# Optimization experiments

Hardware: AMD Instinct MI355X
Metric: run time of the kernel (lower is better)

## Reference

```python
import jax, jax.numpy as jnp
import numpy as np

LAG = 13
B = 32
N = 1200
NUM = 0  # self.num at call time (module starts at the init value)
H = 1.0 / 3.0


def gamma_fn(x):
    # Gamma function valid for positive and negative non-integer args
    # (reflection formula for x<0), elementwise, fp32-safe.
    xp = jnp.where(x > 0, x, jnp.float32(1.0))
    pos = jnp.exp(jax.lax.lgamma(xp))
    xn = jnp.where(x > 0, jnp.float32(0.5), x)
    neg = jnp.pi / (jnp.sin(jnp.pi * xn) * jnp.exp(jax.lax.lgamma(1.0 - xn)))
    return jnp.where(x > 0, pos, neg)


def aggregate(A, WW):
    # Fused form of: repeat_interleave -> view -> mul(WW) -> sum(dim=2) -> tanh(-x)
    # v0[l,b,i,j,e] = A[l,b,i,e]; out[l,b,j,e] = tanh(-sum_i WW[i,j,e]*A[l,b,i,e])
    return jnp.tanh(-jnp.einsum('lbie,ije->lbje', A, WW))


def setup_inputs() -> dict:
    key = jax.random.key(0)
    k = jax.random.split(key, 7)
    A = jax.random.normal(k[0], (LAG - 1, B, N, 1), jnp.float32)
    WW = jax.random.normal(k[1], (N, N, 1), jnp.float32) * 0.03
    train_init = jax.random.uniform(k[2], (B, N, LAG, 2), jnp.float32)
    alpha = jax.random.uniform(k[3], (LAG - 1, 1), jnp.float32) * 0.6 + 0.2
    fract = jax.random.uniform(k[4], (LAG - 1, 1), jnp.float32) * 0.6 + 0.2
    lambd = jax.random.normal(k[5], (LAG - 1, 1, N // 6, 1), jnp.float32) * 0.1
    l = jax.random.normal(k[6], (LAG - 1, 1, N // 6, 1), jnp.float32) * 0.1
    A_y_list = jnp.zeros((12, B, LAG - 1, N, 1), jnp.float32)
    return {"A": A, "WW": WW, "train_init": train_init, "alpha": alpha,
            "fract": fract, "lambd": lambd, "l": l, "A_y_list": A_y_list}


def reference(A, WW, train_init, alpha, fract, lambd, l, A_y_list):
    # __init__-time precomputation of A_N_OLD / A_0_NEW
    A_N_OLD = aggregate(jnp.transpose(train_init[..., :LAG - 1, 1], (2, 0, 1))[..., None], WW)
    A_0_NEW = aggregate(jnp.transpose(train_init[..., 1:LAG, 1], (2, 0, 1))[..., None], WW)

    out = aggregate(A, WW)                                   # [lag-1,B,N,1]
    A_y_list = A_y_list.at[NUM].set(jnp.transpose(out, (1, 0, 2, 3)))

    # D(): the original overwrites num=0 inside D, so only the m=0 GL term
    # survives; binom(fract,0)=Gamma(f+1)/(Gamma(1)Gamma(f+1)).
    binom0 = gamma_fn(fract + 1.0) / (gamma_fn(jnp.ones_like(fract)) * gamma_fn(fract + 1.0))
    sum_GL = A_y_list[0] * binom0[None, :, None, :]          # [B,lag-1,N,1]
    output_final_A = sum_GL / (H ** fract[None, :, None, :])

    # belta_result = sum_{k=0..3} Gamma(a+1)/(Gamma(k+1)Gamma(a-k+1))
    g_a1 = gamma_fn(alpha + 1.0)                             # [lag-1,1]
    belta_result = jnp.zeros((LAG - 1, 1), jnp.float32)
    for kk in range(4):
        kf = jnp.full((LAG - 1, 1), float(kk), jnp.float32)
        belta_result = belta_result + g_a1 / (gamma_fn(kf + 1.0) * gamma_fn(alpha - kf + 1.0))

    tmp1 = g_a1[:, None, None, :]                            # Gamma(a+1), == tmp3
    tmp2 = gamma_fn(jnp.ones((LAG - 1, 1), jnp.float32))[:, None, None, :]   # Gamma(1)=1
    tmp4 = gamma_fn(jnp.full((LAG - 1, 1), 4.0, jnp.float32))[:, None, None, :]  # Gamma(4)=6
    tmp5 = gamma_fn(alpha - 2.0)[:, None, None, :]           # Gamma(a-3+1)

    l_rep = jnp.tile(l, (1, B, 6, 1))                        # [lag-1,B,N,1]
    constant = l_rep * (tmp1 / (tmp2 * tmp1) * A_0_NEW + tmp1 / (tmp4 * tmp5) * A_N_OLD) / H
    constant = jnp.transpose(constant, (1, 0, 2, 3))         # [B,lag-1,N,1]

    lambd_rep = jnp.transpose(jnp.tile(lambd, (1, B, 6, 1)), (1, 0, 2, 3))
    return lambd_rep / belta_result[None, :, None, :] * (2.0 * output_final_A + constant)
```

## Files before the change

kernel.cpp:

```cpp
#include <hip/hip_runtime.h>
#include <math.h>

#define PI_F 3.14159265358979323846f

typedef __attribute__((ext_vector_type(8))) short bh8;
typedef __attribute__((ext_vector_type(4))) float f32x4;

#define LAG1 12
#define BB   32
#define NN   1200
#define MROWS 1152
#define KPAD 1216
#define NPAD 1216

__device__ __forceinline__ unsigned short f2bf(float f) {
    unsigned int u = __float_as_uint(f);
    u = (u + 0x7fffu + ((u >> 16) & 1u)) >> 16;
    return (unsigned short)u;
}

__device__ __forceinline__ float gamma_fn_dev(float x) {
    if (x > 0.0f) return expf(lgammaf(x));
    return PI_F / (sinf(PI_F * x) * expf(lgammaf(1.0f - x)));
}

__global__ void prep_coef(const float* __restrict__ alpha, const float* __restrict__ fract,
                          float* __restrict__ coef) {
    int lag = threadIdx.x;
    if (lag >= LAG1) return;
    float a = alpha[lag], f = fract[lag];
    float ga1 = expf(lgammaf(a + 1.0f));
    float belta = 0.0f;
    const float gk[4] = {1.0f, 1.0f, 2.0f, 6.0f};
    #pragma unroll
    for (int kk = 0; kk < 4; kk++)
        belta += ga1 / (gk[kk] * gamma_fn_dev(a - (float)kk + 1.0f));
    float c2 = ga1 / (6.0f * gamma_fn_dev(a - 2.0f));
    coef[lag]      = 2.0f * powf(3.0f, f);
    coef[12 + lag] = c2;
    coef[24 + lag] = 1.0f / belta;
}

__global__ void prep_X(const float* __restrict__ A, const float* __restrict__ TI,
                       unsigned short* __restrict__ X) {
    int idx = blockIdx.x * 256 + threadIdx.x;
    if (idx >= MROWS * KPAD) return;
    int r = idx / KPAD, k = idx - r * KPAD;
    float v = 0.0f;
    if (k < NN) {
        int g = r / 384, rr = r - g * 384;
        int lag = rr >> 5, b = rr & 31;
        if (g == 0) {
            v = A[rr * NN + k];
        } else {
            int lg = (g == 1) ? lag : (lag + 1);
            v = TI[((b * NN + k) * 13 + lg) * 2 + 1];
        }
    }
    X[idx] = f2bf(v);
}

__global__ void prep_WT(const float* __restrict__ WW, unsigned short* __restrict__ WT) {
    __shared__ float tile[32][33];
    int i0 = blockIdx.y * 32, j0 = blockIdx.x * 32;
    int tx = threadIdx.x, ty = threadIdx.y;
    #pragma unroll
    for (int s = 0; s < 32; s += 8) {
        int i = i0 + ty + s, j = j0 + tx;
        tile[ty + s][tx] = (i < NN && j < NN) ? WW[i * NN + j] : 0.0f;
    }
    __syncthreads();
    #pragma unroll
    for (int s = 0; s < 32; s += 8) {
        int j = j0 + ty + s, i = i0 + tx;
        WT[j * NPAD + i] = f2bf(tile[tx][ty + s]);
    }
}

__global__ __launch_bounds__(256) void gemm_kernel(const unsigned short* __restrict__ X,
                                                   const unsigned short* __restrict__ WT,
                                                   float* __restrict__ T) {
    __shared__ unsigned short As[64 * 40];
    __shared__ unsigned short Bs[64 * 40];
    const int tid  = threadIdx.x;
    const int bm   = blockIdx.x, bn = blockIdx.y;
    const int wave = tid >> 6, lane = tid & 63;
    const int wm   = (wave >> 1) * 32, wn = (wave & 1) * 32;
    const int lrow = tid >> 2;
    const int lcol = (tid & 3) * 8;
    const int l15  = lane & 15;
    const int kq   = (lane >> 4) * 8;

    const unsigned short* gA = X  + (bm * 64 + lrow) * KPAD + lcol;
    const unsigned short* gB = WT + (bn * 64 + lrow) * NPAD + lcol;

    f32x4 acc[2][2] = {};

    for (int k0 = 0; k0 < KPAD; k0 += 32) {
        __syncthreads();
        *(int4*)&As[lrow * 40 + lcol] = *(const int4*)(gA + k0);
        *(int4*)&Bs[lrow * 40 + lcol] = *(const int4*)(gB + k0);
        __syncthreads();
        bh8 a0 = *(const bh8*)&As[(wm +      l15) * 40 + kq];
        bh8 a1 = *(const bh8*)&As[(wm + 16 + l15) * 40 + kq];
        bh8 b0 = *(const bh8*)&Bs[(wn +      l15) * 40 + kq];
        bh8 b1 = *(const bh8*)&Bs[(wn + 16 + l15) * 40 + kq];
        acc[0][0] = __builtin_amdgcn_mfma_f32_16x16x32_bf16(a0, b0, acc[0][0], 0, 0, 0);
        acc[0][1] = __builtin_amdgcn_mfma_f32_16x16x32_bf16(a0, b1, acc[0][1], 0, 0, 0);
        acc[1][0] = __builtin_amdgcn_mfma_f32_16x16x32_bf16(a1, b0, acc[1][0], 0, 0, 0);
        acc[1][1] = __builtin_amdgcn_mfma_f32_16x16x32_bf16(a1, b1, acc[1][1], 0, 0, 0);
    }

    #pragma unroll
    for (int fm = 0; fm < 2; fm++) {
        #pragma unroll
        for (int fn = 0; fn < 2; fn++) {
            #pragma unroll
            for (int r = 0; r < 4; r++) {
                int gm = bm * 64 + wm + fm * 16 + (lane >> 4) * 4 + r;
                int gn = bn * 64 + wn + fn * 16 + l15;
                if (gn < NN) T[gm * NN + gn] = tanhf(-acc[fm][fn][r]);
            }
        }
    }
}

__global__ void epilogue(const float* __restrict__ T, const float* __restrict__ lambd,
                         const float* __restrict__ l, const float* __restrict__ coef,
                         float* __restrict__ out) {
    int idx = blockIdx.x * 256 + threadIdx.x;
    if (idx >= BB * LAG1 * NN) return;
    int j = idx % NN;
    int t = idx / NN;
    int lag = t % LAG1, b = t / LAG1;
    int r = lag * 32 + b;
    float Tout = T[r * NN + j];
    float TN   = T[(384 + r) * NN + j];
    float T0   = T[(768 + r) * NN + j];
    int jm = j % 200;
    float lv  = l[lag * 200 + jm];
    float lam = lambd[lag * 200 + jm];
    float e0 = coef[lag], c2 = coef[12 + lag], ib = coef[24 + lag];
    out[idx] = lam * ib * (e0 * Tout + 3.0f * lv * (T0 + c2 * TN));
}

extern "C" void kernel_launch(void* const* d_in, const int* in_sizes, int n_in,
                              void* d_out, int out_size, void* d_ws, size_t ws_size,
                              hipStream_t stream) {
    const float* A     = (const float*)d_in[0];
    const float* WW    = (const float*)d_in[1];
    const float* TI    = (const float*)d_in[2];
    const float* alpha = (const float*)d_in[3];
    const float* fract = (const float*)d_in[4];
    const float* lambd = (const float*)d_in[5];
    const float* l     = (const float*)d_in[6];
    float* out = (float*)d_out;

    unsigned short* X  = (unsigned short*)d_ws;
    unsigned short* WT = X + MROWS * KPAD;
    float* T    = (float*)(WT + NPAD * NPAD);
    float* coef = T + MROWS * NN;

    prep_coef<<<1, 64, 0, stream>>>(alpha, fract, coef);
    prep_X<<<(MROWS * KPAD + 255) / 256, 256, 0, stream>>>(A, TI, X);
    prep_WT<<<dim3(38, 38), dim3(32, 8), 0, stream>>>(WW, WT);
    gemm_kernel<<<dim3(18, 19), 256, 0, stream>>>(X, WT, T);
    epilogue<<<(BB * LAG1 * NN + 255) / 256, 256, 0, stream>>>(T, lambd, l, coef, out);
}
```

Measured before the change: 125.7 us.

## Fuse prep kernels into one launch and fold epilogue into per-lag GEMM

Merges the three preprocessing kernels into a single block-partitioned launch, reads train_init rows coalesced per (b,i) and writes A rows with vectorized stores. The GEMM is regrouped so that each block handles one lag and holds the three matching 32-row groups (out, A_N_OLD, A_0_NEW), with a 64-wide K step and 6 MFMA accumulators. The coefficient and elementwise epilogue then run inside the GEMM, which removes the intermediate T buffer and two launches. In exchange the grid shrinks to 228 blocks, each doing more work, which may reduce occupancy.

```diff
diff --git a/kernel.cpp b/kernel.cpp
--- a/kernel.cpp
+++ b/kernel.cpp
@@ -9,9 +9,14 @@
 #define LAG1 12
 #define BB   32
 #define NN   1200
-#define MROWS 1152
 #define KPAD 1216
 #define NPAD 1216
+
+#define ROW_I4 (KPAD / 8)
+#define PA_BLK 228
+#define PB_BLK 150
+#define PD_BLK 6
+#define PC_BLK 1444
 
 __device__ __forceinline__ unsigned short f2bf(float f) {
     unsigned int u = __float_as_uint(f);
@@ -24,10 +29,80 @@
     return PI_F / (sinf(PI_F * x) * expf(lgammaf(1.0f - x)));
 }
 
-__global__ void prep_coef(const float* __restrict__ alpha, const float* __restrict__ fract,
-                          float* __restrict__ coef) {
-    int lag = threadIdx.x;
-    if (lag >= LAG1) return;
+__global__ __launch_bounds__(256) void prep_kernel(const float* __restrict__ A,
+                                                   const float* __restrict__ TI,
+                                                   const float* __restrict__ WW,
+                                                   unsigned short* __restrict__ X,
+                                                   unsigned short* __restrict__ WT) {
+    __shared__ float tile[32][33];
+    const int bid = blockIdx.x;
+    const int t = threadIdx.x;
+
+    if (bid < PA_BLK) {
+        int idx = bid * 256 + t;
+        int r = idx / ROW_I4;
+        int c8 = idx - r * ROW_I4;
+        int k = c8 * 8;
+        unsigned short v[8];
+        #pragma unroll
+        for (int u = 0; u < 8; u++) {
+            int kk = k + u;
+            v[u] = (kk < NN) ? f2bf(A[r * NN + kk]) : (unsigned short)0;
+        }
+        *(int4*)&X[r * KPAD + k] = *(int4*)v;
+    } else if (bid < PA_BLK + PB_BLK) {
+        int idx = (bid - PA_BLK) * 256 + t;
+        int b = idx / NN, i = idx - b * NN;
+        const float* p = TI + (size_t)(b * NN + i) * 26 + 1;
+        float vals[13];
+        #pragma unroll
+        for (int lg = 0; lg < 13; lg++) vals[lg] = p[lg * 2];
+        #pragma unroll
+        for (int lag = 0; lag < LAG1; lag++) {
+            X[(384 + lag * 32 + b) * KPAD + i] = f2bf(vals[lag]);
+            X[(768 + lag * 32 + b) * KPAD + i] = f2bf(vals[lag + 1]);
+        }
+    } else if (bid < PA_BLK + PB_BLK + PD_BLK) {
+        int idx = (bid - PA_BLK - PB_BLK) * 256 + t;
+        if (idx < 768 * 2) {
+            int r = idx >> 1, h = idx & 1;
+            int4 z = {0, 0, 0, 0};
+            *(int4*)&X[(384 + r) * KPAD + 1200 + h * 8] = z;
+        }
+    } else {
+        int cb = bid - (PA_BLK + PB_BLK + PD_BLK);
+        int bx = cb % 38, by = cb / 38;
+        int i0 = by * 32, j0 = bx * 32;
+        int tx = t & 31, ty = t >> 5;
+        #pragma unroll
+        for (int s = 0; s < 32; s += 8) {
+            int i = i0 + ty + s, j = j0 + tx;
+            tile[ty + s][tx] = (i < NN && j < NN) ? WW[i * NN + j] : 0.0f;
+        }
+        __syncthreads();
+        #pragma unroll
+        for (int s = 0; s < 32; s += 8) {
+            int j = j0 + ty + s, i = i0 + tx;
+            WT[j * NPAD + i] = f2bf(tile[tx][ty + s]);
+        }
+    }
+}
+
+__global__ __launch_bounds__(256) void gemm_fused(const unsigned short* __restrict__ X,
+                                                  const unsigned short* __restrict__ WT,
+                                                  const float* __restrict__ alpha,
+                                                  const float* __restrict__ fract,
+                                                  const float* __restrict__ lambd,
+                                                  const float* __restrict__ l,
+                                                  float* __restrict__ out) {
+    __shared__ unsigned short Xs[96 * 72];
+    __shared__ unsigned short Bs[64 * 72];
+    const int lag = blockIdx.x;
+    const int bn  = blockIdx.y;
+    const int t = threadIdx.x;
+    const int wave = t >> 6, lane = t & 63;
+    const int l15 = lane & 15, quad = lane >> 4;
+
     float a = alpha[lag], f = fract[lag];
     float ga1 = expf(lgammaf(a + 1.0f));
     float belta = 0.0f;
@@ -35,113 +110,62 @@
     #pragma unroll
     for (int kk = 0; kk < 4; kk++)
         belta += ga1 / (gk[kk] * gamma_fn_dev(a - (float)kk + 1.0f));
-    float c2 = ga1 / (6.0f * gamma_fn_dev(a - 2.0f));
-    coef[lag]      = 2.0f * powf(3.0f, f);
-    coef[12 + lag] = c2;
-    coef[24 + lag] = 1.0f / belta;
-}
+    const float c2 = ga1 / (6.0f * gamma_fn_dev(a - 2.0f));
+    const float e0 = 2.0f * powf(3.0f, f);
+    const float ib = 1.0f / belta;
 
-__global__ void prep_X(const float* __restrict__ A, const float* __restrict__ TI,
-                       unsigned short* __restrict__ X) {
-    int idx = blockIdx.x * 256 + threadIdx.x;
-    if (idx >= MROWS * KPAD) return;
-    int r = idx / KPAD, k = idx - r * KPAD;
-    float v = 0.0f;
-    if (k < NN) {
-        int g = r / 384, rr = r - g * 384;
-        int lag = rr >> 5, b = rr & 31;
-        if (g == 0) {
-            v = A[rr * NN + k];
-        } else {
-            int lg = (g == 1) ? lag : (lag + 1);
-            v = TI[((b * NN + k) * 13 + lg) * 2 + 1];
+    const int n0 = bn * 64;
+    const int j  = n0 + wave * 16 + l15;
+    const int jm = (j < NN) ? (j % 200) : 0;
+    const float lv  = l[lag * 200 + jm];
+    const float lam = lambd[lag * 200 + jm];
+
+    f32x4 acc[6] = {};
+
+    for (int k0 = 0; k0 < KPAD; k0 += 64) {
+        __syncthreads();
+        #pragma unroll
+        for (int u = 0; u < 3; u++) {
+            int idx = t + u * 256;
+            int row = idx >> 3, c8 = idx & 7;
+            int g = row >> 5, w = row & 31;
+            int grow = g * 384 + lag * 32 + w;
+            *(int4*)&Xs[row * 72 + c8 * 8] =
+                *(const int4*)&X[(size_t)grow * KPAD + k0 + c8 * 8];
         }
-    }
-    X[idx] = f2bf(v);
-}
-
-__global__ void prep_WT(const float* __restrict__ WW, unsigned short* __restrict__ WT) {
-    __shared__ float tile[32][33];
-    int i0 = blockIdx.y * 32, j0 = blockIdx.x * 32;
-    int tx = threadIdx.x, ty = threadIdx.y;
-    #pragma unroll
-    for (int s = 0; s < 32; s += 8) {
-        int i = i0 + ty + s, j = j0 + tx;
-        tile[ty + s][tx] = (i < NN && j < NN) ? WW[i * NN + j] : 0.0f;
-    }
-    __syncthreads();
-    #pragma unroll
-    for (int s = 0; s < 32; s += 8) {
-        int j = j0 + ty + s, i = i0 + tx;
-        WT[j * NPAD + i] = f2bf(tile[tx][ty + s]);
-    }
-}
-
-__global__ __launch_bounds__(256) void gemm_kernel(const unsigned short* __restrict__ X,
-                                                   const unsigned short* __restrict__ WT,
-                                                   float* __restrict__ T) {
-    __shared__ unsigned short As[64 * 40];
-    __shared__ unsigned short Bs[64 * 40];
-    const int tid  = threadIdx.x;
-    const int bm   = blockIdx.x, bn = blockIdx.y;
-    const int wave = tid >> 6, lane = tid & 63;
-    const int wm   = (wave >> 1) * 32, wn = (wave & 1) * 32;
-    const int lrow = tid >> 2;
-    const int lcol = (tid & 3) * 8;
-    const int l15  = lane & 15;
-    const int kq   = (lane >> 4) * 8;
-
-    const unsigned short* gA = X  + (bm * 64 + lrow) * KPAD + lcol;
-    const unsigned short* gB = WT + (bn * 64 + lrow) * NPAD + lcol;
-
-    f32x4 acc[2][2] = {};
-
-    for (int k0 = 0; k0 < KPAD; k0 += 32) {
+        #pragma unroll
+        for (int u = 0; u < 2; u++) {
+            int idx = t + u * 256;
+            int row = idx >> 3, c8 = idx & 7;
+            *(int4*)&Bs[row * 72 + c8 * 8] =
+                *(const int4*)&WT[(size_t)(n0 + row) * NPAD + k0 + c8 * 8];
+        }
         __syncthreads();
-        *(int4*)&As[lrow * 40 + lcol] = *(const int4*)(gA + k0);
-        *(int4*)&Bs[lrow * 40 + lcol] = *(const int4*)(gB + k0);
-        __syncthreads();
-        bh8 a0 = *(const bh8*)&As[(wm +      l15) * 40 + kq];
-        bh8 a1 = *(const bh8*)&As[(wm + 16 + l15) * 40 + kq];
-        bh8 b0 = *(const bh8*)&Bs[(wn +      l15) * 40 + kq];
-        bh8 b1 = *(const bh8*)&Bs[(wn + 16 + l15) * 40 + kq];
-        acc[0][0] = __builtin_amdgcn_mfma_f32_16x16x32_bf16(a0, b0, acc[0][0], 0, 0, 0);
-        acc[0][1] = __builtin_amdgcn_mfma_f32_16x16x32_bf16(a0, b1, acc[0][1], 0, 0, 0);
-        acc[1][0] = __builtin_amdgcn_mfma_f32_16x16x32_bf16(a1, b0, acc[1][0], 0, 0, 0);
-        acc[1][1] = __builtin_amdgcn_mfma_f32_16x16x32_bf16(a1, b1, acc[1][1], 0, 0, 0);
-    }
-
-    #pragma unroll
-    for (int fm = 0; fm < 2; fm++) {
         #pragma unroll
-        for (int fn = 0; fn < 2; fn++) {
+        for (int kh = 0; kh < 2; kh++) {
+            bh8 bfrag = *(const bh8*)&Bs[(wave * 16 + l15) * 72 + kh * 32 + quad * 8];
             #pragma unroll
-            for (int r = 0; r < 4; r++) {
-                int gm = bm * 64 + wm + fm * 16 + (lane >> 4) * 4 + r;
-                int gn = bn * 64 + wn + fn * 16 + l15;
-                if (gn < NN) T[gm * NN + gn] = tanhf(-acc[fm][fn][r]);
+            for (int fm = 0; fm < 6; fm++) {
+                bh8 afrag = *(const bh8*)&Xs[(fm * 16 + l15) * 72 + kh * 32 + quad * 8];
+                acc[fm] = __builtin_amdgcn_mfma_f32_16x16x32_bf16(afrag, bfrag, acc[fm], 0, 0, 0);
             }
         }
     }
-}
 
-__global__ void epilogue(const float* __restrict__ T, const float* __restrict__ lambd,
-                         const float* __restrict__ l, const float* __restrict__ coef,
-                         float* __restrict__ out) {
-    int idx = blockIdx.x * 256 + threadIdx.x;
-    if (idx >= BB * LAG1 * NN) return;
-    int j = idx % NN;
-    int t = idx / NN;
-    int lag = t % LAG1, b = t / LAG1;
-    int r = lag * 32 + b;
-    float Tout = T[r * NN + j];
-    float TN   = T[(384 + r) * NN + j];
-    float T0   = T[(768 + r) * NN + j];
-    int jm = j % 200;
-    float lv  = l[lag * 200 + jm];
-    float lam = lambd[lag * 200 + jm];
-    float e0 = coef[lag], c2 = coef[12 + lag], ib = coef[24 + lag];
-    out[idx] = lam * ib * (e0 * Tout + 3.0f * lv * (T0 + c2 * TN));
+    if (j < NN) {
+        #pragma unroll
+        for (int fp = 0; fp < 2; fp++) {
+            #pragma unroll
+            for (int r = 0; r < 4; r++) {
+                int b = fp * 16 + quad * 4 + r;
+                float tA = tanhf(-acc[fp][r]);
+                float tN = tanhf(-acc[2 + fp][r]);
+                float t0 = tanhf(-acc[4 + fp][r]);
+                out[(b * LAG1 + lag) * NN + j] =
+                    lam * ib * (e0 * tA + 3.0f * lv * (t0 + c2 * tN));
+            }
+        }
+    }
 }
 
 extern "C" void kernel_launch(void* const* d_in, const int* in_sizes, int n_in,
@@ -157,13 +181,8 @@
     float* out = (float*)d_out;
 
     unsigned short* X  = (unsigned short*)d_ws;
-    unsigned short* WT = X + MROWS * KPAD;
-    float* T    = (float*)(WT + NPAD * NPAD);
-    float* coef = T + MROWS * NN;
+    unsigned short* WT = X + 1152 * KPAD;
 
-    prep_coef<<<1, 64, 0, stream>>>(alpha, fract, coef);
-    prep_X<<<(MROWS * KPAD + 255) / 256, 256, 0, stream>>>(A, TI, X);
-    prep_WT<<<dim3(38, 38), dim3(32, 8), 0, stream>>>(WW, WT);
-    gemm_kernel<<<dim3(18, 19), 256, 0, stream>>>(X, WT, T);
-    epilogue<<<(BB * LAG1 * NN + 255) / 256, 256, 0, stream>>>(T, lambd, l, coef, out);
+    prep_kernel<<<PA_BLK + PB_BLK + PD_BLK + PC_BLK, 256, 0, stream>>>(A, TI, WW, X, WT);
+    gemm_fused<<<dim3(LAG1, 19), 256, 0, stream>>>(X, WT, alpha, fract, lambd, l, out);
 }
```

After: 132.1 us. 1.05x slower.
